# Kernel optimization log

Measured on AMD Instinct MI355X. Metric: run time of the kernel, lower is better.

## Reference

```python
import jax, jax.numpy as jnp
import numpy as np

EPS = 1e-6
CHUNK = 64
GATE_LOGIT_NORMALIZER = 16.0
NUM_HEADS = 4


def _rms(x, w):
    return x * jax.lax.rsqrt(jnp.mean(x * x, axis=-1, keepdims=True) + EPS) * w


def _gla_chunk(q, k, v, glog, num_heads):
    # q,k: [B,T,Dk] v: [B,T,Dv] glog: [B,T,Dk] (log decay, <=0)
    B, T, Dk = q.shape
    Dv = v.shape[-1]
    dk, dv = Dk // num_heads, Dv // num_heads
    Nc = T // CHUNK

    def split(x, d):
        # [B,T,H*d] -> [B,H,Nc,C,d]
        return x.reshape(B, T, num_heads, d).transpose(0, 2, 1, 3).reshape(B, num_heads, Nc, CHUNK, d)

    q, k, v, g = split(q, dk), split(k, dk), split(v, dv), split(glog, dk)
    b = jnp.cumsum(g, axis=3)  # inclusive cumulative log-decay within chunk
    scale = dk ** -0.5
    qe = q * jnp.exp(b) * scale

    # intra-chunk: A[t,s] = sum_d q_t k_s exp(b_t - b_s), causal (t>=s)
    mask = jnp.tril(jnp.ones((CHUNK, CHUNK), dtype=bool))
    A = jnp.einsum('bhncd,bhnsd->bhncs', qe, k * jnp.exp(-b))
    A = jnp.where(mask, A, 0.0)
    o_intra = jnp.einsum('bhncs,bhnsd->bhncd', A, v)

    # inter-chunk recurrence over state S: [B,H,dk,dv]
    def step(S, xs):
        qe_c, k_c, v_c, b_c = xs  # [B,H,C,*]
        blast = b_c[:, :, -1, :]                      # [B,H,dk]
        o_inter = jnp.einsum('bhcd,bhde->bhce', qe_c, S)
        kd = k_c * jnp.exp(blast[:, :, None, :] - b_c)
        S_new = S * jnp.exp(blast)[..., None] + jnp.einsum('bhcd,bhce->bhde', kd, v_c)
        return S_new, o_inter

    S0 = jnp.zeros((B, num_heads, dk, dv), q.dtype)
    xs = tuple(jnp.moveaxis(t, 2, 0) for t in (qe, k, v, b))
    _, o_inter = jax.lax.scan(step, S0, xs)
    o = o_intra + jnp.moveaxis(o_inter, 0, 2)  # [B,H,Nc,C,dv]
    return o.reshape(B, num_heads, T, dv).transpose(0, 2, 1, 3)  # [B,T,H,dv]


def setup_inputs() -> dict:
    key = jax.random.key(0)
    ks = jax.random.split(key, 12)
    B, T, Hs = 4, 2048, 1024
    Dk, Dv, I, R = 512, 1024, 2816, 16
    p = lambda k, s: jax.random.normal(k, s, jnp.float32) * 0.02
    return {
        'hidden_states': jax.random.normal(ks[0], (B, T, Hs), jnp.float32),
        'attn_norm_w': jnp.ones((Hs,), jnp.float32),
        'Wq': p(ks[1], (Hs, Dk)), 'Wk': p(ks[2], (Hs, Dk)), 'Wv': p(ks[3], (Hs, Dv)),
        'Wg': p(ks[4], (Hs, Dv)),
        'Wgk1': p(ks[5], (Hs, R)), 'Wgk2': p(ks[6], (R, Dk)), 'bgk2': jnp.zeros((Dk,), jnp.float32),
        'gnorm_w': jnp.ones((Dv // NUM_HEADS,), jnp.float32),
        'Wo': p(ks[7], (Dv, Hs)),
        'mlp_norm_w': jnp.ones((Hs,), jnp.float32),
        'W_gate': p(ks[8], (Hs, I)), 'W_up': p(ks[9], (Hs, I)), 'W_down': p(ks[10], (I, Hs)),
    }


def reference(hidden_states, attn_norm_w, Wq, Wk, Wv, Wg, Wgk1, Wgk2, bgk2,
              gnorm_w, Wo, mlp_norm_w, W_gate, W_up, W_down):
    x = hidden_states
    h = _rms(x, attn_norm_w)
    q, k, v = h @ Wq, h @ Wk, h @ Wv
    glog = jax.nn.log_sigmoid(h @ Wgk1 @ Wgk2 + bgk2) / GATE_LOGIT_NORMALIZER
    o = _gla_chunk(q, k, v, glog, NUM_HEADS)          # [B,T,H,dv]
    g_out = (h @ Wg).reshape(o.shape)
    o = _rms(o, gnorm_w) * (g_out * jax.nn.sigmoid(g_out))  # per-head RMSNorm + swish gate
    attn_out = o.reshape(x.shape[0], x.shape[1], -1) @ Wo
    # fused residual RMSNorm
    x2 = attn_out + x
    n = _rms(x2, mlp_norm_w)
    mlp = (jax.nn.silu(n @ W_gate) * (n @ W_up)) @ W_down
    return x2 + mlp
```

## Files before the change

kernel.cpp:

```cpp
#include <hip/hip_runtime.h>

typedef unsigned short u16;
typedef __attribute__((ext_vector_type(8))) short bf8_t;
typedef __attribute__((ext_vector_type(4))) float f4_t;

#define MFMA_B16(a,b,c) __builtin_amdgcn_mfma_f32_16x16x32_bf16(a,b,c,0,0,0)

#define TOKS 8192
#define HS   1024
#define DKTOT 512
#define DVTOT 1024
#define IM   2816

constexpr size_t OFF_WQT    = 0;
constexpr size_t OFF_WKT    = OFF_WQT    + (size_t)DKTOT*HS*2;
constexpr size_t OFF_WVT    = OFF_WKT    + (size_t)DKTOT*HS*2;
constexpr size_t OFF_WGT    = OFF_WVT    + (size_t)DVTOT*HS*2;
constexpr size_t OFF_WOT    = OFF_WGT    + (size_t)DVTOT*HS*2;
constexpr size_t OFF_WGATET = OFF_WOT    + (size_t)HS*DVTOT*2;
constexpr size_t OFF_WUPT   = OFF_WGATET + (size_t)IM*HS*2;
constexpr size_t OFF_WDOWNT = OFF_WUPT   + (size_t)IM*HS*2;
constexpr size_t OFF_QE     = OFF_WDOWNT + (size_t)HS*IM*2;
constexpr size_t OFF_CTST   = OFF_QE     + (size_t)TOKS*DKTOT*2;
constexpr size_t OFF_DEC    = OFF_CTST   + (size_t)512*256*128*2;
constexpr size_t OFF_R1     = OFF_DEC    + (size_t)512*128*4;
constexpr size_t OFF_QKB    = OFF_R1;
constexpr size_t OFF_GLOG   = OFF_QKB    + (size_t)TOKS*1024*2;
constexpr size_t OFF_VT     = OFF_GLOG   + (size_t)TOKS*DKTOT*4;
constexpr size_t OFF_UP     = OFF_R1;
constexpr size_t OFF_R3     = OFF_R1 + 50331648;
constexpr size_t OFF_H      = OFF_R3;
constexpr size_t OFF_OI     = OFF_R3;
constexpr size_t OFF_N2     = OFF_R3;
constexpr size_t OFF_R4     = OFF_R3 + 16777216;
constexpr size_t OFF_GO     = OFF_R4;
constexpr size_t OFF_OG     = OFF_R4;
constexpr size_t WS_NEED    = OFF_R4 + 16777216;

__device__ __forceinline__ u16 f2bf(float f){
  union{ float f; unsigned u; } x; x.f = f;
  unsigned r = x.u + 0x7FFFu + ((x.u >> 16) & 1u);
  return (u16)(r >> 16);
}
__device__ __forceinline__ float bf2f(u16 u){
  union{ unsigned u; float f; } x; x.u = ((unsigned)u) << 16; return x.f;
}
__device__ __forceinline__ void gl_lds16(const void* g, void* l){
  __builtin_amdgcn_global_load_lds(
      (const __attribute__((address_space(1))) unsigned int*)g,
      (__attribute__((address_space(3))) unsigned int*)l, 16, 0, 0);
}
__device__ __forceinline__ int swz128(int row, int cb){ return row*128 + (cb ^ ((row & 7)  << 4)); }
__device__ __forceinline__ int swz256(int row, int cb){ return row*256 + (cb ^ ((row & 15) << 4)); }

__device__ __forceinline__ void xcd_map(int gx, int gy, int& bm, int& bn){
  const int i   = blockIdx.y*gx + blockIdx.x;
  const int cpx = (gx*gy) >> 3;
  const int j   = (i & 7)*cpx + (i >> 3);
  const int k   = j / (gx*8);
  const int jl  = j - k*(gx*8);
  bn = jl >> 3;
  bm = k*8 + (jl & 7);
}

struct TransAll {
  const float* src[8];
  u16* dst[8];
  int K[8];
  int N[8];
  int end[8];
};

__global__ __launch_bounds__(256) void k_transpose_all(TransAll ta)
{
  __shared__ float tile[64][65];
  const int flat = blockIdx.x;
  int seg = 0, start = 0;
  #pragma unroll
  for(int j=0;j<8;j++){
    if(flat >= ta.end[j]){ seg = j+1; start = ta.end[j]; }
  }
  const float* W = ta.src[seg];
  u16* Wt = ta.dst[seg];
  const int K = ta.K[seg], N = ta.N[seg];
  const int local = flat - start;
  const int tilesX = N >> 6;
  const int n0 = (local % tilesX)*64, k0 = (local / tilesX)*64;
  const int tx = threadIdx.x & 63, tg = threadIdx.x >> 6;
  #pragma unroll
  for(int i=0;i<16;i++){
    int kr = tg*16 + i;
    tile[kr][tx] = W[(size_t)(k0+kr)*N + n0 + tx];
  }
  __syncthreads();
  #pragma unroll
  for(int i=0;i<16;i++){
    int nr = tg*16 + i;
    Wt[(size_t)(n0+nr)*K + k0 + tx] = f2bf(tile[tx][nr]);
  }
}

__global__ __launch_bounds__(256) void k_rmsnorm(
    const float* __restrict__ X, const float* __restrict__ W, u16* __restrict__ H)
{
  __shared__ float red[4];
  const size_t row = blockIdx.x;
  const int t = threadIdx.x;
  const float4 v = ((const float4*)(X + row*1024))[t];
  float ss = v.x*v.x + v.y*v.y + v.z*v.z + v.w*v.w;
  #pragma unroll
  for(int m=32;m>=1;m>>=1) ss += __shfl_xor(ss, m, 64);
  if((t & 63) == 0) red[t >> 6] = ss;
  __syncthreads();
  ss = red[0] + red[1] + red[2] + red[3];
  const float rs = rsqrtf(ss*(1.f/1024.f) + 1e-6f);
  const float4 w = ((const float4*)W)[t];
  ushort4 o;
  o.x = f2bf(v.x*rs*w.x);
  o.y = f2bf(v.y*rs*w.y);
  o.z = f2bf(v.z*rs*w.z);
  o.w = f2bf(v.w*rs*w.w);
  ((ushort4*)H)[row*256 + t] = o;
}

__global__ __launch_bounds__(256) void k_rms_glog(
    const float* __restrict__ X, const float* __restrict__ W, u16* __restrict__ H,
    const float* __restrict__ W1, const float* __restrict__ W2,
    const float* __restrict__ bias, float* __restrict__ G)
{
  __shared__ float hs[1024];
  __shared__ float red2[16][17];
  __shared__ float rr[16];
  __shared__ float red[4];
  const size_t row = blockIdx.x;
  const int t = threadIdx.x;
  const float4 v = ((const float4*)(X + row*1024))[t];
  float ss = v.x*v.x + v.y*v.y + v.z*v.z + v.w*v.w;
  #pragma unroll
  for(int m=32;m>=1;m>>=1) ss += __shfl_xor(ss, m, 64);
  if((t & 63) == 0) red[t >> 6] = ss;
  __syncthreads();
  ss = red[0] + red[1] + red[2] + red[3];
  const float rs = rsqrtf(ss*(1.f/1024.f) + 1e-6f);
  const float4 w = ((const float4*)W)[t];
  const float h0 = v.x*rs*w.x, h1 = v.y*rs*w.y, h2 = v.z*rs*w.z, h3 = v.w*rs*w.w;
  ushort4 o; o.x = f2bf(h0); o.y = f2bf(h1); o.z = f2bf(h2); o.w = f2bf(h3);
  ((ushort4*)H)[row*256 + t] = o;
  hs[t*4+0] = h0; hs[t*4+1] = h1; hs[t*4+2] = h2; hs[t*4+3] = h3;
  __syncthreads();

  const int r = t & 15, c = t >> 4;
  float acc = 0.f;
  #pragma unroll
  for(int j=0;j<64;j++){
    int k = c*64 + ((j + c) & 63);
    acc += hs[k] * W1[(size_t)k*16 + r];
  }
  red2[c][r] = acc;
  __syncthreads();
  if(t < 16){
    float s2 = 0.f;
    #pragma unroll
    for(int cc=0;cc<16;cc++) s2 += red2[cc][t];
    rr[t] = s2;
  }
  __syncthreads();
  #pragma unroll
  for(int dd=0;dd<2;dd++){
    int dcol = t + dd*256;
    float z = bias[dcol];
    #pragma unroll
    for(int j=0;j<16;j++) z += rr[j]*W2[j*512 + dcol];
    float ls = fminf(z, 0.f) - log1pf(__expf(-fabsf(z)));
    G[row*512 + dcol] = ls * 0.0625f;
  }
}

enum { E_BF16=1, E_ADDF32=2, E_SILUMUL=3, E_QKVG=5 };

template<int EPI>
__global__ __launch_bounds__(512, 2) void k_gemm8(
    const u16* __restrict__ A, const u16* __restrict__ Bt,
    void* __restrict__ Cp, const void* __restrict__ aux,
    int M, int N, int K)
{
  __shared__ __align__(16) u16 lds[3*24576];
  const int t = threadIdx.x;
  const int wv = t >> 6, ln = t & 63, lr = ln & 15, lg = ln >> 4;
  const int wm = wv >> 2, wn = wv & 3;
  int bm, bn; xcd_map(gridDim.x, gridDim.y, bm, bn);
  const int m0 = bm*128, n0 = bn*256;
  const int NT = K >> 6;

  const int sr = t >> 3;
  const int sc = ((t & 7)*16 ^ ((sr & 7) << 4)) >> 1;
  const u16* Asrc = A  + (size_t)(m0 + sr)*K + sc;
  const u16* Bsrc = Bt + (size_t)(n0 + sr)*K + sc;

  auto stage = [&](int T){
    const int b = T % 3;
    const size_t ko = (size_t)T * 64;
    u16* dA = lds + b*24576 + wv*512;
    u16* dB = lds + b*24576 + 8192 + wv*512;
    gl_lds16(Asrc + ko,                    dA);
    gl_lds16(Asrc + (size_t)64*K + ko,     dA + 4096);
    #pragma unroll
    for(int j=0;j<4;j++)
      gl_lds16(Bsrc + (size_t)(j*64)*K + ko, dB + j*4096);
  };

  f4_t acc[4][4];
  #pragma unroll
  for(int i=0;i<4;i++)
    #pragma unroll
    for(int j=0;j<4;j++) acc[i][j] = f4_t{0.f,0.f,0.f,0.f};

  const int rA = wm*64 + lr;
  const int rB = wn*64 + lr;
  const int cxor = (lr & 7) << 4;

  auto compute = [&](int b){
    const char* La = (const char*)(lds + b*24576);
    const char* Lb = La + 16384;
    #pragma unroll
    for(int kk=0;kk<2;++kk){
      const int cb = (kk*64 + lg*16) ^ cxor;
      bf8_t af[4], bfr[4];
      #pragma unroll
      for(int m=0;m<4;m++) af[m]  = *(const bf8_t*)(La + (rA + m*16)*128 + cb);
      #pragma unroll
      for(int n=0;n<4;n++) bfr[n] = *(const bf8_t*)(Lb + (rB + n*16)*128 + cb);
      __builtin_amdgcn_s_setprio(1);
      #pragma unroll
      for(int m=0;m<4;m++)
        #pragma unroll
        for(int n=0;n<4;n++)
          acc[m][n] = MFMA_B16(af[m], bfr[n], acc[m][n]);
      __builtin_amdgcn_s_setprio(0);
    }
  };

  stage(0);
  stage(1);

  for(int T=0; T<NT-1; ++T){
    asm volatile("s_waitcnt vmcnt(6)" ::: "memory");
    __builtin_amdgcn_s_barrier();
    asm volatile("" ::: "memory");
    __builtin_amdgcn_sched_barrier(0);
    if(T+2 < NT) stage(T+2);
    compute(T % 3);
  }
  asm volatile("s_waitcnt vmcnt(0)" ::: "memory");
  __builtin_amdgcn_s_barrier();
  asm volatile("" ::: "memory");
  __builtin_amdgcn_sched_barrier(0);
  compute((NT-1) % 3);

  #pragma unroll
  for(int m=0;m<4;m++){
    #pragma unroll
    for(int n=0;n<4;n++){
      const int row0 = m0 + wm*64 + m*16 + lg*4;
      const int col  = n0 + wn*64 + n*16 + lr;
      if constexpr(EPI==E_QKVG){
        char* wsb = (char*)Cp;
        if(n0 < 1024){
          u16* dst = (u16*)(wsb + OFF_QKB);
          #pragma unroll
          for(int r=0;r<4;r++) dst[(size_t)(row0+r)*1024 + col] = f2bf(acc[m][n][r]);
        } else if(n0 < 2048){
          u16* dst = (u16*)(wsb + OFF_VT);
          ushort4 u;
          u.x = f2bf(acc[m][n][0]); u.y = f2bf(acc[m][n][1]);
          u.z = f2bf(acc[m][n][2]); u.w = f2bf(acc[m][n][3]);
          *(ushort4*)(dst + (size_t)(col-1024)*TOKS + row0) = u;
        } else {
          u16* dst = (u16*)(wsb + OFF_GO);
          #pragma unroll
          for(int r=0;r<4;r++) dst[(size_t)(row0+r)*1024 + (col-2048)] = f2bf(acc[m][n][r]);
        }
      } else {
        #pragma unroll
        for(int r=0;r<4;r++){
          const size_t idx = (size_t)(row0+r)*N + col;
          float v = acc[m][n][r];
          if constexpr(EPI==E_BF16) ((u16*)Cp)[idx] = f2bf(v);
          else if constexpr(EPI==E_ADDF32) ((float*)Cp)[idx] = v + ((const float*)aux)[idx];
          else if constexpr(EPI==E_SILUMUL){
            float u = bf2f(((const u16*)aux)[idx]);
            ((u16*)Cp)[idx] = f2bf(u * v / (1.f + __expf(-v)));
          }
        }
      }
    }
  }
}

__global__ __launch_bounds__(256) void k_gla_a(
    const u16* __restrict__ QK,
    const u16* __restrict__ VT, const float* __restrict__ G,
    u16* __restrict__ QE, u16* __restrict__ OI,
    u16* __restrict__ CT, float* __restrict__ DEC)
{
  __shared__ __align__(16) u16 qe_s[64*128];
  __shared__ __align__(16) u16 ke_s[64*128];
  __shared__ __align__(16) u16 kd_s[128*64];
  __shared__ __align__(16) u16 a_s [64*64];
  __shared__ float ps_s[2][128];

  const int bid = blockIdx.x;
  const int nc = bid & 31, hh = (bid >> 5) & 3, bb = bid >> 7;
  const int bh = bb*4 + hh;
  const int tok0 = bb*2048 + nc*64;
  const int t = threadIdx.x;
  const size_t cbase = (size_t)(bh*32 + nc);

  {
    const int d = t & 127;
    const int half = t >> 7;
    const int col = hh*128 + d;
    const int i0 = half*32;
    float g[32];
    float psum = 0.f;
    #pragma unroll
    for(int i=0;i<32;i++){
      g[i] = G[(size_t)(tok0+i0+i)*512 + col];
      psum += g[i];
    }
    ps_s[half][d] = psum;
    __syncthreads();
    const float cum0  = half ? ps_s[0][d] : 0.f;
    const float blast = ps_s[0][d] + ps_s[1][d];
    if(half == 0) DEC[cbase*128 + d] = __expf(blast);
    float cum = cum0;
    #pragma unroll
    for(int i=0;i<32;i++){
      cum += g[i];
      const int tok = tok0 + i0 + i;
      float qv = bf2f(QK[(size_t)tok*1024 + col]);
      float kv = bf2f(QK[(size_t)tok*1024 + 512 + col]);
      float qe = qv * __expf(cum) * 0.08838834764831845f;
      float ke = kv * __expf(-cum);
      float kd = kv * __expf(blast - cum);
      *(u16*)((char*)qe_s + swz256(i0+i, d*2)) = f2bf(qe);
      *(u16*)((char*)ke_s + swz256(i0+i, d*2)) = f2bf(ke);
      *(u16*)((char*)kd_s + swz128(d, (i0+i)*2)) = f2bf(kd);
      QE[(cbase*64 + i0+i)*128 + d] = f2bf(qe);
    }
  }
  __syncthreads();

  const int wv = t >> 6, ln = t & 63, lr = ln & 15, lg = ln >> 4;

  bf8_t aq[4];
  #pragma unroll
  for(int ks=0;ks<4;ks++)
    aq[ks] = *(const bf8_t*)((const char*)qe_s + swz256(wv*16 + lr, ks*64 + lg*16));
  #pragma unroll
  for(int n=0;n<4;n++){
    f4_t accA = f4_t{0.f,0.f,0.f,0.f};
    #pragma unroll
    for(int ks=0;ks<4;ks++){
      bf8_t bk = *(const bf8_t*)((const char*)ke_s + swz256(n*16 + lr, ks*64 + lg*16));
      accA = MFMA_B16(aq[ks], bk, accA);
    }
    #pragma unroll
    for(int r=0;r<4;r++){
      int i = wv*16 + lg*4 + r;
      int s = n*16 + lr;
      float v = (s <= i) ? accA[r] : 0.f;
      *(u16*)((char*)a_s + swz128(i, s*2)) = f2bf(v);
    }
  }
  __syncthreads();

  bf8_t af[2], kf[2][2];
  #pragma unroll
  for(int ks=0;ks<2;ks++)
    af[ks] = *(const bf8_t*)((const char*)a_s + swz128(wv*16 + lr, ks*64 + lg*16));
  #pragma unroll
  for(int p=0;p<2;p++)
    #pragma unroll
    for(int ks=0;ks<2;ks++)
      kf[p][ks] = *(const bf8_t*)((const char*)kd_s + swz128((2*wv+p)*16 + lr, ks*64 + lg*16));

  #pragma unroll 4
  for(int ne=0; ne<16; ne++){
    bf8_t vf[2];
    #pragma unroll
    for(int ks=0;ks<2;ks++)
      vf[ks] = *(const bf8_t*)(VT + (size_t)(hh*256 + ne*16 + lr)*8192 + tok0 + ks*32 + lg*8);
    f4_t ao = f4_t{0.f,0.f,0.f,0.f};
    ao = MFMA_B16(af[0], vf[0], ao);
    ao = MFMA_B16(af[1], vf[1], ao);
    #pragma unroll
    for(int r=0;r<4;r++)
      OI[(cbase*64 + wv*16 + lg*4 + r)*256 + ne*16 + lr] = f2bf(ao[r]);
    f4_t c0 = f4_t{0.f,0.f,0.f,0.f}, c1 = f4_t{0.f,0.f,0.f,0.f};
    c0 = MFMA_B16(kf[0][0], vf[0], c0);
    c0 = MFMA_B16(kf[0][1], vf[1], c0);
    c1 = MFMA_B16(kf[1][0], vf[0], c1);
    c1 = MFMA_B16(kf[1][1], vf[1], c1);
    u16* dst = CT + (cbase*256 + ne*16 + lr)*128;
    ushort4 u0, u1;
    u0.x=f2bf(c0[0]); u0.y=f2bf(c0[1]); u0.z=f2bf(c0[2]); u0.w=f2bf(c0[3]);
    u1.x=f2bf(c1[0]); u1.y=f2bf(c1[1]); u1.z=f2bf(c1[2]); u1.w=f2bf(c1[3]);
    *(ushort4*)(dst + (2*wv+0)*16 + lg*4) = u0;
    *(ushort4*)(dst + (2*wv+1)*16 + lg*4) = u1;
  }
}

__global__ __launch_bounds__(256) void k_scan(
    u16* __restrict__ CTST, const float* __restrict__ DEC)
{
  const int idx = blockIdx.x*256 + threadIdx.x;
  const int d = idx & 127;
  const int e = (idx >> 7) & 255;
  const int bh = idx >> 15;
  float s = 0.f;
  for(int n=0;n<32;n++){
    const size_t off = ((size_t)(bh*32 + n)*256 + e)*128 + d;
    float c = bf2f(CTST[off]);
    CTST[off] = f2bf(s);
    s = s * DEC[(bh*32+n)*128 + d] + c;
  }
}

__global__ __launch_bounds__(256) void k_gla_c(
    const u16* __restrict__ QE, const u16* __restrict__ ST,
    const u16* __restrict__ OI, const u16* __restrict__ GO,
    const float* __restrict__ GW, u16* __restrict__ OG)
{
  const int bid = blockIdx.x;
  const int nc = bid & 31, hh = (bid >> 5) & 3, bb = bid >> 7;
  const int bh = bb*4 + hh;
  const int tok0 = bb*2048 + nc*64;
  const int t = threadIdx.x;
  const int wv = t >> 6, ln = t & 63, lr = ln & 15, lg = ln >> 4;
  const size_t cbase = (size_t)(bh*32 + nc);

  bf8_t qf[4];
  #pragma unroll
  for(int ks=0;ks<4;ks++)
    qf[ks] = *(const bf8_t*)(QE + (cbase*64 + wv*16 + lr)*128 + ks*32 + lg*8);

  f4_t acc[16];
  #pragma unroll
  for(int ne=0;ne<16;ne++){
    f4_t a = f4_t{0.f,0.f,0.f,0.f};
    #pragma unroll
    for(int ks=0;ks<4;ks++){
      bf8_t sf = *(const bf8_t*)(ST + (cbase*256 + ne*16 + lr)*128 + ks*32 + lg*8);
      a = MFMA_B16(qf[ks], sf, a);
    }
    acc[ne] = a;
  }

  float vals[16][4];
  float ss[4] = {0.f,0.f,0.f,0.f};
  #pragma unroll
  for(int ne=0;ne<16;ne++)
    #pragma unroll
    for(int r=0;r<4;r++){
      float v = acc[ne][r] + bf2f(OI[(cbase*64 + wv*16 + lg*4 + r)*256 + ne*16 + lr]);
      vals[ne][r] = v;
      ss[r] += v*v;
    }
  #pragma unroll
  for(int r=0;r<4;r++){
    ss[r] += __shfl_xor(ss[r], 1, 64);
    ss[r] += __shfl_xor(ss[r], 2, 64);
    ss[r] += __shfl_xor(ss[r], 4, 64);
    ss[r] += __shfl_xor(ss[r], 8, 64);
  }
  float rs[4];
  #pragma unroll
  for(int r=0;r<4;r++) rs[r] = rsqrtf(ss[r]*(1.f/256.f) + 1e-6f);

  #pragma unroll
  for(int ne=0;ne<16;ne++)
    #pragma unroll
    for(int r=0;r<4;r++){
      int i = wv*16 + lg*4 + r;
      int e = ne*16 + lr;
      const size_t idx = (size_t)(tok0+i)*1024 + hh*256 + e;
      float gg = bf2f(GO[idx]);
      float sg = gg / (1.f + __expf(-gg));
      OG[idx] = f2bf(vals[ne][r]*rs[r]*GW[e]*sg);
    }
}

extern "C" void kernel_launch(void* const* d_in, const int* in_sizes, int n_in,
                              void* d_out, int out_size, void* d_ws, size_t ws_size,
                              hipStream_t stream) {
  (void)in_sizes; (void)n_in; (void)out_size;
  if (ws_size < WS_NEED) return;

  const float* x       = (const float*)d_in[0];
  const float* attn_w  = (const float*)d_in[1];
  const float* Wq      = (const float*)d_in[2];
  const float* Wk      = (const float*)d_in[3];
  const float* Wv      = (const float*)d_in[4];
  const float* Wg      = (const float*)d_in[5];
  const float* Wgk1    = (const float*)d_in[6];
  const float* Wgk2    = (const float*)d_in[7];
  const float* bgk2    = (const float*)d_in[8];
  const float* gnw     = (const float*)d_in[9];
  const float* Wo      = (const float*)d_in[10];
  const float* mlpw    = (const float*)d_in[11];
  const float* Wgate   = (const float*)d_in[12];
  const float* Wup     = (const float*)d_in[13];
  const float* Wdown   = (const float*)d_in[14];
  char* ws = (char*)d_ws;

  u16*   wqt   = (u16*)(ws + OFF_WQT);
  u16*   wkt   = (u16*)(ws + OFF_WKT);
  u16*   wvt   = (u16*)(ws + OFF_WVT);
  u16*   wgt   = (u16*)(ws + OFF_WGT);
  u16*   wot   = (u16*)(ws + OFF_WOT);
  u16*   wgatet= (u16*)(ws + OFF_WGATET);
  u16*   wupt  = (u16*)(ws + OFF_WUPT);
  u16*   wdownt= (u16*)(ws + OFF_WDOWNT);
  u16*   qeb   = (u16*)(ws + OFF_QE);
  u16*   ctst  = (u16*)(ws + OFF_CTST);
  float* decb  = (float*)(ws + OFF_DEC);
  u16*   qkb   = (u16*)(ws + OFF_QKB);
  float* glogb = (float*)(ws + OFF_GLOG);
  u16*   vtb   = (u16*)(ws + OFF_VT);
  u16*   upb   = (u16*)(ws + OFF_UP);
  u16*   hb    = (u16*)(ws + OFF_H);
  u16*   oib   = (u16*)(ws + OFF_OI);
  u16*   n2b   = (u16*)(ws + OFF_N2);
  u16*   gob   = (u16*)(ws + OFF_GO);
  u16*   ogb   = (u16*)(ws + OFF_OG);
  float* x2b   = (float*)d_out;

  dim3 blk(256);
  dim3 blk8(512);

  TransAll ta;
  ta.src[0]=Wq;    ta.dst[0]=wqt;    ta.K[0]=HS;  ta.N[0]=DKTOT;
  ta.src[1]=Wk;    ta.dst[1]=wkt;    ta.K[1]=HS;  ta.N[1]=DKTOT;
  ta.src[2]=Wv;    ta.dst[2]=wvt;    ta.K[2]=HS;  ta.N[2]=DVTOT;
  ta.src[3]=Wg;    ta.dst[3]=wgt;    ta.K[3]=HS;  ta.N[3]=DVTOT;
  ta.src[4]=Wo;    ta.dst[4]=wot;    ta.K[4]=DVTOT; ta.N[4]=HS;
  ta.src[5]=Wgate; ta.dst[5]=wgatet; ta.K[5]=HS;  ta.N[5]=IM;
  ta.src[6]=Wup;   ta.dst[6]=wupt;   ta.K[6]=HS;  ta.N[6]=IM;
  ta.src[7]=Wdown; ta.dst[7]=wdownt; ta.K[7]=IM;  ta.N[7]=HS;
  {
    int cum = 0;
    for(int j=0;j<8;j++){ cum += (ta.N[j]>>6)*(ta.K[j]>>6); ta.end[j] = cum; }
  }
  k_transpose_all<<<3136, blk, 0, stream>>>(ta);

  k_rms_glog<<<TOKS, blk, 0, stream>>>(x, attn_w, hb, Wgk1, Wgk2, bgk2, glogb);
  k_gemm8<E_QKVG><<<dim3(12, 64), blk8, 0, stream>>>(hb, wqt, ws, nullptr, TOKS, 3072, HS);

  k_gla_a<<<512, blk, 0, stream>>>(qkb, vtb, glogb, qeb, oib, ctst, decb);
  k_scan <<<2048, blk, 0, stream>>>(ctst, decb);
  k_gla_c<<<512, blk, 0, stream>>>(qeb, ctst, oib, gob, gnw, ogb);

  k_gemm8<E_ADDF32><<<dim3(4, 64), blk8, 0, stream>>>(ogb, wot, x2b, x, TOKS, HS, DVTOT);

  k_rmsnorm<<<TOKS, blk, 0, stream>>>(x2b, mlpw, n2b);
  k_gemm8<E_BF16>   <<<dim3(11, 64), blk8, 0, stream>>>(n2b, wupt,   upb, nullptr, TOKS, IM, HS);
  k_gemm8<E_SILUMUL><<<dim3(11, 64), blk8, 0, stream>>>(n2b, wgatet, upb, upb,     TOKS, IM, HS);
  k_gemm8<E_ADDF32> <<<dim3(4, 64),  blk8, 0, stream>>>(upb, wdownt, x2b, x2b,     TOKS, HS, IM);
}
```

Before: 418.8 us.

## Add 256x256-tile GEMM kernel with double-buffered LDS pipeline for QKVG and MLP-up

Introduces a new GEMM kernel that computes a 256x256 output tile per 512-thread block, with each wave covering 128x64. It uses a two-buffer, 128KB LDS pipeline that interleaves half-tile global-to-LDS loads with MFMA phases, separated by barriers. The kernel replaces the 128-row-tile GEMM for the QKVG projection and the up/gate MLP projections, halving the grid's M dimension, to raise arithmetic intensity and reduce global traffic per FLOP. The cost is more accumulator registers and LDS per block, which can lower occupancy, and fewer blocks for load balancing across CUs. The 256-row tiling only works because the row count is a multiple of 256.

Result: slower. 448.1 us (+7.0%).

```diff
diff --git a/kernel.cpp b/kernel.cpp
--- a/kernel.cpp
+++ b/kernel.cpp
@@ -262,6 +262,124 @@
     #pragma unroll
     for(int n=0;n<4;n++){
       const int row0 = m0 + wm*64 + m*16 + lg*4;
+      const int col  = n0 + wn*64 + n*16 + lr;
+      #pragma unroll
+      for(int r=0;r<4;r++){
+        const size_t idx = (size_t)(row0+r)*N + col;
+        float v = acc[m][n][r];
+        if constexpr(EPI==E_BF16) ((u16*)Cp)[idx] = f2bf(v);
+        else if constexpr(EPI==E_ADDF32) ((float*)Cp)[idx] = v + ((const float*)aux)[idx];
+        else if constexpr(EPI==E_SILUMUL){
+          float u = bf2f(((const u16*)aux)[idx]);
+          ((u16*)Cp)[idx] = f2bf(u * v / (1.f + __expf(-v)));
+        }
+      }
+    }
+  }
+}
+
+template<int EPI>
+__global__ __launch_bounds__(512, 2) void k_gemm10(
+    const u16* __restrict__ A, const u16* __restrict__ Bt,
+    void* __restrict__ Cp, const void* __restrict__ aux,
+    int M, int N, int K)
+{
+  __shared__ __align__(16) char lds[131072];
+  const int t = threadIdx.x;
+  const int wv = t >> 6, ln = t & 63, lr = ln & 15, lg = ln >> 4;
+  const int wm = wv >> 2, wn = wv & 3;
+  int bm, bn; xcd_map(gridDim.x, gridDim.y, bm, bn);
+  const int m0 = bm*256, n0 = bn*256;
+  const int NT = K >> 6;
+
+  const int sl   = t & 7;
+  const int pgl  = (t >> 3) & 7;
+  const int unsw = 16*(sl ^ pgl);
+  const int rloc = ((t >> 3) << 1) + (unsw >> 6);
+  const int cole = (unsw & 63) >> 1;
+  const u16* Asrc = A  + (size_t)(m0 + rloc)*K + cole;
+  const u16* Bsrc = Bt + (size_t)(n0 + rloc)*K + cole;
+
+  auto STAGE = [&](int tt, int mat, int kh){
+    if(tt >= NT) return;
+    const size_t ko = (size_t)tt*64 + kh*32;
+    const u16* s = mat ? Bsrc : Asrc;
+    char* d = lds + ((tt & 1) << 16) + (mat << 15) + (kh << 14) + (wv << 10);
+    gl_lds16(s + ko,                  d);
+    gl_lds16(s + (size_t)128*K + ko,  d + 8192);
+  };
+
+  f4_t acc[8][4];
+  #pragma unroll
+  for(int i=0;i<8;i++)
+    #pragma unroll
+    for(int j=0;j<4;j++) acc[i][j] = f4_t{0.f,0.f,0.f,0.f};
+
+  bf8_t bfr[4];
+  auto LDB = [&](int buf, int kk){
+    #pragma unroll
+    for(int n=0;n<4;n++){
+      const int R = wn*64 + n*16 + lr;
+      const int pg = R >> 1;
+      const int off = (buf<<16) + 32768 + (kk<<14) + pg*128
+                    + ((((R&1)<<6) | (lg<<4)) ^ ((pg&7)<<4));
+      bfr[n] = *(const bf8_t*)(lds + off);
+    }
+  };
+  auto MFMAPH = [&](int buf, int kk, int mh){
+    bf8_t af[4];
+    #pragma unroll
+    for(int m=0;m<4;m++){
+      const int R = wm*128 + (mh*4+m)*16 + lr;
+      const int pg = R >> 1;
+      const int off = (buf<<16) + (kk<<14) + pg*128
+                    + ((((R&1)<<6) | (lg<<4)) ^ ((pg&7)<<4));
+      af[m] = *(const bf8_t*)(lds + off);
+    }
+    asm volatile("s_waitcnt lgkmcnt(0)" ::: "memory");
+    __builtin_amdgcn_sched_barrier(0);
+    __builtin_amdgcn_s_setprio(1);
+    #pragma unroll
+    for(int m=0;m<4;m++)
+      #pragma unroll
+      for(int n=0;n<4;n++)
+        acc[mh*4+m][n] = MFMA_B16(af[m], bfr[n], acc[mh*4+m][n]);
+    __builtin_amdgcn_s_setprio(0);
+  };
+
+  #define GBAR do{ asm volatile("" ::: "memory"); __builtin_amdgcn_s_barrier(); \
+                   asm volatile("" ::: "memory"); }while(0)
+
+  STAGE(0,1,0); STAGE(0,0,0); STAGE(0,1,1); STAGE(0,0,1);
+  STAGE(1,1,0); STAGE(1,0,0); STAGE(1,1,1);
+  asm volatile("s_waitcnt vmcnt(6)" ::: "memory");
+  GBAR;
+
+  const int NI = NT >> 1;
+  for(int j=0; j<NI; ++j){
+    const int t1 = 2*j+1;
+    const bool last = (j == NI-1);
+    LDB(0,0); STAGE(t1,0,1);          MFMAPH(0,0,0); GBAR;
+    STAGE(t1+1,1,0);                  MFMAPH(0,0,1); GBAR;
+    LDB(0,1); STAGE(t1+1,0,0);        MFMAPH(0,1,0); GBAR;
+    STAGE(t1+1,1,1);                  MFMAPH(0,1,1);
+    if(last) asm volatile("s_waitcnt vmcnt(0)" ::: "memory");
+    else     asm volatile("s_waitcnt vmcnt(6)" ::: "memory");
+    GBAR;
+    LDB(1,0); STAGE(t1+1,0,1);        MFMAPH(1,0,0); GBAR;
+    STAGE(t1+2,1,0);                  MFMAPH(1,0,1); GBAR;
+    LDB(1,1); STAGE(t1+2,0,0);        MFMAPH(1,1,0); GBAR;
+    STAGE(t1+2,1,1);                  MFMAPH(1,1,1);
+    if(!last){ asm volatile("s_waitcnt vmcnt(6)" ::: "memory"); }
+    GBAR;
+  }
+  #undef GBAR
+
+  #pragma unroll
+  for(int m=0;m<8;m++){
+    #pragma unroll
+    for(int n=0;n<4;n++){
+      const int row0 = m0 + wm*128 + m*16 + lg*4;
       const int col  = n0 + wn*64 + n*16 + lr;
       if constexpr(EPI==E_QKVG){
         char* wsb = (char*)Cp;
@@ -555,7 +673,7 @@
   k_transpose_all<<<3136, blk, 0, stream>>>(ta);
 
   k_rms_glog<<<TOKS, blk, 0, stream>>>(x, attn_w, hb, Wgk1, Wgk2, bgk2, glogb);
-  k_gemm8<E_QKVG><<<dim3(12, 64), blk8, 0, stream>>>(hb, wqt, ws, nullptr, TOKS, 3072, HS);
+  k_gemm10<E_QKVG><<<dim3(12, 32), blk8, 0, stream>>>(hb, wqt, ws, nullptr, TOKS, 3072, HS);
 
   k_gla_a<<<512, blk, 0, stream>>>(qkb, vtb, glogb, qeb, oib, ctst, decb);
   k_scan <<<2048, blk, 0, stream>>>(ctst, decb);
@@ -564,7 +682,7 @@
   k_gemm8<E_ADDF32><<<dim3(4, 64), blk8, 0, stream>>>(ogb, wot, x2b, x, TOKS, HS, DVTOT);
 
   k_rmsnorm<<<TOKS, blk, 0, stream>>>(x2b, mlpw, n2b);
-  k_gemm8<E_BF16>   <<<dim3(11, 64), blk8, 0, stream>>>(n2b, wupt,   upb, nullptr, TOKS, IM, HS);
-  k_gemm8<E_SILUMUL><<<dim3(11, 64), blk8, 0, stream>>>(n2b, wgatet, upb, upb,     TOKS, IM, HS);
-  k_gemm8<E_ADDF32> <<<dim3(4, 64),  blk8, 0, stream>>>(upb, wdownt, x2b, x2b,     TOKS, HS, IM);
-}
+  k_gemm10<E_BF16>   <<<dim3(11, 32), blk8, 0, stream>>>(n2b, wupt,   upb, nullptr, TOKS, IM, HS);
+  k_gemm10<E_SILUMUL><<<dim3(11, 32), blk8, 0, stream>>>(n2b, wgatet, upb, upb,     TOKS, IM, HS);
+  k_gemm8<E_ADDF32>  <<<dim3(4, 64),  blk8, 0, stream>>>(upb, wdownt, x2b, x2b,     TOKS, HS, IM);
+}
```

## Fuse MLP up and gate GEMMs into one dual-accumulator kernel

Applied to the files above, without the earlier changes.

Replaces the separate up-projection GEMM and the gate GEMM with one kernel that loads the activation tile once and accumulates both up and gate products from two weight tiles, applying SiLU-multiply in the epilogue. This removes a full read of the normalized activations, the bf16 write and read of the intermediate up result, and one kernel launch. The N tile shrinks to 128 per weight with two accumulator sets, which changes register pressure and the grid shape (22x64).

Measured after the change: 407.6 us. -2.7%, faster.

```diff
diff --git a/kernel.cpp b/kernel.cpp
--- a/kernel.cpp
+++ b/kernel.cpp
@@ -176,7 +176,7 @@
   }
 }
 
-enum { E_BF16=1, E_ADDF32=2, E_SILUMUL=3, E_QKVG=5 };
+enum { E_BF16=1, E_ADDF32=2, E_QKVG=5 };
 
 template<int EPI>
 __global__ __launch_bounds__(512, 2) void k_gemm8(
@@ -287,11 +287,111 @@
           float v = acc[m][n][r];
           if constexpr(EPI==E_BF16) ((u16*)Cp)[idx] = f2bf(v);
           else if constexpr(EPI==E_ADDF32) ((float*)Cp)[idx] = v + ((const float*)aux)[idx];
-          else if constexpr(EPI==E_SILUMUL){
-            float u = bf2f(((const u16*)aux)[idx]);
-            ((u16*)Cp)[idx] = f2bf(u * v / (1.f + __expf(-v)));
-          }
         }
+      }
+    }
+  }
+}
+
+__global__ __launch_bounds__(512, 2) void k_gemm8_ug(
+    const u16* __restrict__ A, const u16* __restrict__ Bu,
+    const u16* __restrict__ Bg, u16* __restrict__ Cp,
+    int M, int N, int K)
+{
+  __shared__ __align__(16) u16 lds[3*24576];
+  const int t = threadIdx.x;
+  const int wv = t >> 6, ln = t & 63, lr = ln & 15, lg = ln >> 4;
+  const int wm = wv >> 2, wn = wv & 3;
+  int bm, bn; xcd_map(gridDim.x, gridDim.y, bm, bn);
+  const int m0 = bm*128, n0 = bn*128;
+  const int NT = K >> 6;
+
+  const int sr = t >> 3;
+  const int sc = ((t & 7)*16 ^ ((sr & 7) << 4)) >> 1;
+  const u16* Asrc  = A  + (size_t)(m0 + sr)*K + sc;
+  const u16* Busrc = Bu + (size_t)(n0 + sr)*K + sc;
+  const u16* Bgsrc = Bg + (size_t)(n0 + sr)*K + sc;
+
+  auto stage = [&](int T){
+    const int b = T % 3;
+    const size_t ko = (size_t)T * 64;
+    u16* dA  = lds + b*24576 +         wv*512;
+    u16* dBu = lds + b*24576 + 8192  + wv*512;
+    u16* dBg = lds + b*24576 + 16384 + wv*512;
+    gl_lds16(Asrc  + ko,                 dA);
+    gl_lds16(Asrc  + (size_t)64*K + ko,  dA  + 4096);
+    gl_lds16(Busrc + ko,                 dBu);
+    gl_lds16(Busrc + (size_t)64*K + ko,  dBu + 4096);
+    gl_lds16(Bgsrc + ko,                 dBg);
+    gl_lds16(Bgsrc + (size_t)64*K + ko,  dBg + 4096);
+  };
+
+  f4_t accU[4][2], accG[4][2];
+  #pragma unroll
+  for(int i=0;i<4;i++)
+    #pragma unroll
+    for(int j=0;j<2;j++){ accU[i][j] = f4_t{0.f,0.f,0.f,0.f}; accG[i][j] = f4_t{0.f,0.f,0.f,0.f}; }
+
+  const int rA = wm*64 + lr;
+  const int rB = wn*32 + lr;
+  const int cxor = (lr & 7) << 4;
+
+  auto compute = [&](int b){
+    const char* La  = (const char*)(lds + b*24576);
+    const char* Lbu = La + 16384;
+    const char* Lbg = La + 32768;
+    #pragma unroll
+    for(int kk=0;kk<2;++kk){
+      const int cb = (kk*64 + lg*16) ^ cxor;
+      bf8_t af[4], bu[2], bg[2];
+      #pragma unroll
+      for(int m=0;m<4;m++) af[m] = *(const bf8_t*)(La  + (rA + m*16)*128 + cb);
+      #pragma unroll
+      for(int n=0;n<2;n++){
+        bu[n] = *(const bf8_t*)(Lbu + (rB + n*16)*128 + cb);
+        bg[n] = *(const bf8_t*)(Lbg + (rB + n*16)*128 + cb);
+      }
+      __builtin_amdgcn_s_setprio(1);
+      #pragma unroll
+      for(int m=0;m<4;m++)
+        #pragma unroll
+        for(int n=0;n<2;n++){
+          accU[m][n] = MFMA_B16(af[m], bu[n], accU[m][n]);
+          accG[m][n] = MFMA_B16(af[m], bg[n], accG[m][n]);
+        }
+      __builtin_amdgcn_s_setprio(0);
+    }
+  };
+
+  stage(0);
+  stage(1);
+
+  for(int T=0; T<NT-1; ++T){
+    asm volatile("s_waitcnt vmcnt(6)" ::: "memory");
+    __builtin_amdgcn_s_barrier();
+    asm volatile("" ::: "memory");
+    __builtin_amdgcn_sched_barrier(0);
+    if(T+2 < NT) stage(T+2);
+    compute(T % 3);
+  }
+  asm volatile("s_waitcnt vmcnt(0)" ::: "memory");
+  __builtin_amdgcn_s_barrier();
+  asm volatile("" ::: "memory");
+  __builtin_amdgcn_sched_barrier(0);
+  compute((NT-1) % 3);
+
+  #pragma unroll
+  for(int m=0;m<4;m++){
+    #pragma unroll
+    for(int n=0;n<2;n++){
+      const int row0 = m0 + wm*64 + m*16 + lg*4;
+      const int col  = n0 + wn*32 + n*16 + lr;
+      #pragma unroll
+      for(int r=0;r<4;r++){
+        const size_t idx = (size_t)(row0+r)*N + col;
+        float uv = accU[m][n][r];
+        float gv = accG[m][n][r];
+        Cp[idx] = f2bf(uv * gv / (1.f + __expf(-gv)));
       }
     }
   }
@@ -564,7 +664,6 @@
   k_gemm8<E_ADDF32><<<dim3(4, 64), blk8, 0, stream>>>(ogb, wot, x2b, x, TOKS, HS, DVTOT);
 
   k_rmsnorm<<<TOKS, blk, 0, stream>>>(x2b, mlpw, n2b);
-  k_gemm8<E_BF16>   <<<dim3(11, 64), blk8, 0, stream>>>(n2b, wupt,   upb, nullptr, TOKS, IM, HS);
-  k_gemm8<E_SILUMUL><<<dim3(11, 64), blk8, 0, stream>>>(n2b, wgatet, upb, upb,     TOKS, IM, HS);
-  k_gemm8<E_ADDF32> <<<dim3(4, 64),  blk8, 0, stream>>>(upb, wdownt, x2b, x2b,     TOKS, HS, IM);
-}
+  k_gemm8_ug<<<dim3(22, 64), blk8, 0, stream>>>(n2b, wupt, wgatet, upb, TOKS, IM, HS);
+  k_gemm8<E_ADDF32><<<dim3(4, 64), blk8, 0, stream>>>(upb, wdownt, x2b, x2b, TOKS, HS, IM);
+}
```
